# Kernel optimization log

Measured on AMD Instinct MI355X. Metric: run time of the kernel, lower is better.

Reference implementation:

```python
import jax, jax.numpy as jnp
import numpy as np
from jax import lax

N_NODES = 100000
N_EDGES = 6400000


def setup_inputs() -> dict:
    key = jax.random.key(0)
    k1, k2, k3, k4 = jax.random.split(key, 4)
    values = jax.random.uniform(k1, (N_NODES,), dtype=jnp.float32)
    edge_weights = jax.random.normal(k2, (N_EDGES,), dtype=jnp.float32)
    neighbor_idx = jax.random.randint(k3, (N_EDGES,), 0, N_NODES, dtype=jnp.int64 if jax.config.jax_enable_x64 else jnp.int32)
    segment_ids = jnp.sort(jax.random.randint(k4, (N_EDGES,), 0, N_NODES, dtype=jnp.int64 if jax.config.jax_enable_x64 else jnp.int32))
    return {
        "values": values,
        "edge_weights": edge_weights,
        "neighbor_idx": neighbor_idx,
        "segment_ids": segment_ids,
        "n_times": 3,
    }


def reference(values, edge_weights, neighbor_idx, segment_ids, n_times):
    # One forward_once: for each node i, new[i] = sigmoid(sum_{e: dst(e)=i} w_e * values[src(e)])
    # (per-node Linear(num_links, 1, bias=False) + Sigmoid, flattened over the ragged edge list)
    n_nodes = values.shape[0]

    def step(v, _):
        msgs = edge_weights * v[neighbor_idx]                      # [n_edges]
        agg = jax.ops.segment_sum(msgs, segment_ids, num_segments=n_nodes)
        return jax.nn.sigmoid(agg), None

    out, _ = lax.scan(step, values, None, length=int(n_times))
    return out
```

## Files before the change

kernel.cpp:

```cpp
#include <hip/hip_runtime.h>
#include <hip/hip_bf16.h>

#define BLK    512
#define EPT    8
#define CHUNK  12288
#define NPASS  9
#define CAP    (NPASS * CHUNK)
#define ROUNDS 3
#define SLOTS  640

__device__ __forceinline__ ushort f32_to_bf16_rne(float f) {
    unsigned u = __float_as_uint(f);
    unsigned r = (u + 0x7fffu + ((u >> 16) & 1u)) >> 16;
    return (ushort)r;
}

__global__ __launch_bounds__(BLK) void ppgcn_step(const ushort* __restrict__ vb,
                                                  const float* __restrict__ w,
                                                  const int* __restrict__ idx,
                                                  const int* __restrict__ seg,
                                                  float* __restrict__ acc,
                                                  int n_edges, int n_nodes) {
    __shared__ __align__(16) ushort chunk[2][CHUNK];
    __shared__ float slots[SLOTS];
    __shared__ int s_first, s_last;

    const int tid = threadIdx.x;
    const long long bstart = (long long)blockIdx.x * (BLK * EPT);
    const long long base   = bstart + (long long)tid * EPT;

    int ii[EPT]; float ww[EPT]; int ss[EPT];

    if (base + EPT <= (long long)n_edges) {
        const int4*   ip = reinterpret_cast<const int4*>(idx + base);
        const float4* wp = reinterpret_cast<const float4*>(w + base);
        const int4*   sp = reinterpret_cast<const int4*>(seg + base);
        #pragma unroll
        for (int q = 0; q < EPT / 4; ++q) {
            int4 a = ip[q]; float4 b = wp[q]; int4 c = sp[q];
            ii[4*q+0]=a.x; ii[4*q+1]=a.y; ii[4*q+2]=a.z; ii[4*q+3]=a.w;
            ww[4*q+0]=b.x; ww[4*q+1]=b.y; ww[4*q+2]=b.z; ww[4*q+3]=b.w;
            ss[4*q+0]=c.x; ss[4*q+1]=c.y; ss[4*q+2]=c.z; ss[4*q+3]=c.w;
        }
    } else {
        #pragma unroll
        for (int j = 0; j < EPT; ++j) {
            long long e = base + j;
            bool v = e < (long long)n_edges;
            ii[j] = v ? idx[e] : 0x7fffffff;
            ww[j] = v ? w[e]   : 0.0f;
            ss[j] = v ? seg[e] : 0x7fffffff;
        }
    }

    for (int s = tid; s < SLOTS; s += BLK) slots[s] = 0.0f;
    if (tid == 0) s_first = ss[0];
    {
        long long lastE = ((bstart + BLK * EPT) < (long long)n_edges ?
                           (bstart + BLK * EPT) : (long long)n_edges) - 1;
        int rel   = (int)(lastE - bstart);
        int owner = rel / EPT;
        int jl    = rel % EPT;
        if (tid == owner) s_last = ss[jl];
    }

    float g[EPT];
    #pragma unroll
    for (int j = 0; j < EPT; ++j) g[j] = 0.0f;

    {
        const char* gsrc = (const char*)vb;
        char* ldst = (char*)chunk[0];
        #pragma unroll
        for (int rr = 0; rr < ROUNDS; ++rr) {
            int off = (rr * BLK + tid) * 16;
            __builtin_amdgcn_global_load_lds(
                (const __attribute__((address_space(1))) void*)(gsrc + off),
                (__attribute__((address_space(3))) void*)(ldst + off),
                16, 0, 0);
        }
    }
    __syncthreads();
    const int first = s_first;

    int cur = 0;
    for (int p = 0; p < NPASS; ++p) {
        if (p + 1 < NPASS) {
            const char* gsrc = (const char*)vb + (size_t)(p + 1) * (CHUNK * 2);
            char* ldst = (char*)chunk[cur ^ 1];
            #pragma unroll
            for (int rr = 0; rr < ROUNDS; ++rr) {
                int off = (rr * BLK + tid) * 16;
                __builtin_amdgcn_global_load_lds(
                    (const __attribute__((address_space(1))) void*)(gsrc + off),
                    (__attribute__((address_space(3))) void*)(ldst + off),
                    16, 0, 0);
            }
        }

        const unsigned lo = (unsigned)(p * CHUNK);
        const ushort* cbuf = chunk[cur];
        #pragma unroll
        for (int j = 0; j < EPT; ++j) {
            unsigned rel = (unsigned)ii[j] - lo;
            if (rel < (unsigned)CHUNK) {
                unsigned u = (unsigned)cbuf[rel] << 16;
                g[j] = ww[j] * __uint_as_float(u);
            }
        }

        __syncthreads();
        cur ^= 1;
    }

    {
        float run = g[0]; int cn = ss[0];
        #pragma unroll
        for (int j = 1; j < EPT; ++j) {
            if (ss[j] != cn) {
                if ((unsigned)cn < (unsigned)n_nodes) {
                    unsigned rs = (unsigned)(cn - first);
                    if (rs < (unsigned)SLOTS) atomicAdd(&slots[rs], run);
                    else                      unsafeAtomicAdd(&acc[cn], run);
                }
                cn = ss[j]; run = g[j];
            } else {
                run += g[j];
            }
        }
        if ((unsigned)cn < (unsigned)n_nodes) {
            unsigned rs = (unsigned)(cn - first);
            if (rs < (unsigned)SLOTS) atomicAdd(&slots[rs], run);
            else                      unsafeAtomicAdd(&acc[cn], run);
        }
    }
    __syncthreads();

    {
        const int last = s_last;
        const int span = last - first;
        for (int s = tid; s <= span && s < SLOTS; s += BLK) {
            float v = slots[s];
            int node = first + s;
            if (s == 0 || node == last) unsafeAtomicAdd(&acc[node], v);
            else                        acc[node] = v;
        }
    }
}

__global__ __launch_bounds__(256) void ppgcn_convert(const float* __restrict__ src,
                                                     ushort* __restrict__ dst,
                                                     int n, int cap) {
    int i = blockIdx.x * 256 + threadIdx.x;
    if (i < cap) dst[i] = (i < n) ? f32_to_bf16_rne(src[i]) : (ushort)0;
}

__global__ __launch_bounds__(256) void ppgcn_sigmoid(float* __restrict__ acc,
                                                     ushort* __restrict__ bfout,
                                                     float* __restrict__ fout,
                                                     int n, int cap, int write_f32) {
    int i = blockIdx.x * 256 + threadIdx.x;
    if (i >= cap) return;
    if (i < n) {
        float a = acc[i];
        float s = 1.0f / (1.0f + expf(-a));
        bfout[i] = f32_to_bf16_rne(s);
        if (write_f32) fout[i] = s;
        acc[i] = 0.0f;
    } else {
        bfout[i] = 0;
    }
}

extern "C" void kernel_launch(void* const* d_in, const int* in_sizes, int n_in,
                              void* d_out, int out_size, void* d_ws, size_t ws_size,
                              hipStream_t stream) {
    const float* values       = (const float*)d_in[0];
    const float* edge_weights = (const float*)d_in[1];
    const int*   neighbor_idx = (const int*)d_in[2];
    const int*   segment_ids  = (const int*)d_in[3];

    const int n_nodes = in_sizes[0];
    const int n_edges = in_sizes[1];

    char* ws = (char*)d_ws;
    size_t abytes = ((size_t)n_nodes * sizeof(float) + 255) & ~(size_t)255;
    size_t vbytes = ((size_t)CAP * sizeof(ushort) + 255) & ~(size_t)255;
    float*  acc = (float*)ws;
    ushort* vb0 = (ushort*)(ws + abytes);
    ushort* vb1 = (ushort*)(ws + abytes + vbytes);
    ushort* vb2 = (ushort*)(ws + abytes + 2 * vbytes);
    float*  out = (float*)d_out;

    hipMemsetAsync(acc, 0, (size_t)n_nodes * sizeof(float), stream);

    int eblocks = (int)(((long long)n_edges + BLK * EPT - 1) / (BLK * EPT));
    int cblocks = (CAP + 255) / 256;

    ppgcn_convert<<<cblocks, 256, 0, stream>>>(values, vb0, n_nodes, CAP);

    ppgcn_step<<<eblocks, BLK, 0, stream>>>(vb0, edge_weights, neighbor_idx,
                                            segment_ids, acc, n_edges, n_nodes);
    ppgcn_sigmoid<<<cblocks, 256, 0, stream>>>(acc, vb1, out, n_nodes, CAP, 0);

    ppgcn_step<<<eblocks, BLK, 0, stream>>>(vb1, edge_weights, neighbor_idx,
                                            segment_ids, acc, n_edges, n_nodes);
    ppgcn_sigmoid<<<cblocks, 256, 0, stream>>>(acc, vb2, out, n_nodes, CAP, 0);

    ppgcn_step<<<eblocks, BLK, 0, stream>>>(vb2, edge_weights, neighbor_idx,
                                            segment_ids, acc, n_edges, n_nodes);
    ppgcn_sigmoid<<<cblocks, 256, 0, stream>>>(acc, vb0, out, n_nodes, CAP, 1);
}
```

Baseline: 132.1 us.

## Use smaller chunks with triple-buffered LDS prefetch and vmcnt-based waits

Shrinks the staged bf16 value chunk from 12288 to 4096 entries and switches from double to triple buffering, prefetching two chunks ahead. Each thread now issues one async global-to-LDS load per pass. A pass waits on the vmcnt counter plus a raw s_barrier instead of a full __syncthreads. Total LDS per block drops, which lets more blocks reside per CU (launch bounds now ask for 8), at the cost of 25 passes and barriers instead of 9.

Measured after the change: 183.6 us. 39.0% more time.

```diff
diff --git a/kernel.cpp b/kernel.cpp
--- a/kernel.cpp
+++ b/kernel.cpp
@@ -3,10 +3,10 @@
 
 #define BLK    512
 #define EPT    8
-#define CHUNK  12288
-#define NPASS  9
+#define CHUNK  4096
+#define NBUF   3
+#define NPASS  25
 #define CAP    (NPASS * CHUNK)
-#define ROUNDS 3
 #define SLOTS  640
 
 __device__ __forceinline__ ushort f32_to_bf16_rne(float f) {
@@ -15,13 +15,13 @@
     return (ushort)r;
 }
 
-__global__ __launch_bounds__(BLK) void ppgcn_step(const ushort* __restrict__ vb,
-                                                  const float* __restrict__ w,
-                                                  const int* __restrict__ idx,
-                                                  const int* __restrict__ seg,
-                                                  float* __restrict__ acc,
-                                                  int n_edges, int n_nodes) {
-    __shared__ __align__(16) ushort chunk[2][CHUNK];
+__global__ __launch_bounds__(BLK, 8) void ppgcn_step(const ushort* __restrict__ vb,
+                                                     const float* __restrict__ w,
+                                                     const int* __restrict__ idx,
+                                                     const int* __restrict__ seg,
+                                                     float* __restrict__ acc,
+                                                     int n_edges, int n_nodes) {
+    __shared__ __align__(16) ushort chunk[NBUF][CHUNK];
     __shared__ float slots[SLOTS];
     __shared__ int s_first, s_last;
 
@@ -68,38 +68,42 @@
     #pragma unroll
     for (int j = 0; j < EPT; ++j) g[j] = 0.0f;
 
-    {
-        const char* gsrc = (const char*)vb;
-        char* ldst = (char*)chunk[0];
-        #pragma unroll
-        for (int rr = 0; rr < ROUNDS; ++rr) {
-            int off = (rr * BLK + tid) * 16;
-            __builtin_amdgcn_global_load_lds(
-                (const __attribute__((address_space(1))) void*)(gsrc + off),
-                (__attribute__((address_space(3))) void*)(ldst + off),
-                16, 0, 0);
-        }
+    const int my_off = tid * 16;
+
+    {
+        const char* g0 = (const char*)vb + my_off;
+        const char* g1 = (const char*)vb + (size_t)(CHUNK * 2) + my_off;
+        __builtin_amdgcn_global_load_lds(
+            (const __attribute__((address_space(1))) void*)g0,
+            (__attribute__((address_space(3))) void*)((char*)chunk[0] + my_off),
+            16, 0, 0);
+        __builtin_amdgcn_global_load_lds(
+            (const __attribute__((address_space(1))) void*)g1,
+            (__attribute__((address_space(3))) void*)((char*)chunk[1] + my_off),
+            16, 0, 0);
     }
     __syncthreads();
     const int first = s_first;
 
-    int cur = 0;
     for (int p = 0; p < NPASS; ++p) {
-        if (p + 1 < NPASS) {
-            const char* gsrc = (const char*)vb + (size_t)(p + 1) * (CHUNK * 2);
-            char* ldst = (char*)chunk[cur ^ 1];
-            #pragma unroll
-            for (int rr = 0; rr < ROUNDS; ++rr) {
-                int off = (rr * BLK + tid) * 16;
-                __builtin_amdgcn_global_load_lds(
-                    (const __attribute__((address_space(1))) void*)(gsrc + off),
-                    (__attribute__((address_space(3))) void*)(ldst + off),
-                    16, 0, 0);
-            }
+        if (p > 0) {
+            if (p == NPASS - 1) asm volatile("s_waitcnt vmcnt(0)" ::: "memory");
+            else                asm volatile("s_waitcnt vmcnt(1)" ::: "memory");
+            __builtin_amdgcn_s_barrier();
+            __builtin_amdgcn_sched_barrier(0);
+        }
+
+        if (p + 2 < NPASS) {
+            const char* gs = (const char*)vb + (size_t)(p + 2) * (CHUNK * 2) + my_off;
+            char* ld = (char*)chunk[(p + 2) % NBUF] + my_off;
+            __builtin_amdgcn_global_load_lds(
+                (const __attribute__((address_space(1))) void*)gs,
+                (__attribute__((address_space(3))) void*)ld,
+                16, 0, 0);
         }
 
         const unsigned lo = (unsigned)(p * CHUNK);
-        const ushort* cbuf = chunk[cur];
+        const ushort* cbuf = chunk[p % NBUF];
         #pragma unroll
         for (int j = 0; j < EPT; ++j) {
             unsigned rel = (unsigned)ii[j] - lo;
@@ -108,9 +112,6 @@
                 g[j] = ww[j] * __uint_as_float(u);
             }
         }
-
-        __syncthreads();
-        cur ^= 1;
     }
 
     {
```

## Replace LDS-staged bf16 value chunks with direct fp32 global gathers

Applied to the files above, without the earlier changes.

Drops the per-block loop that streamed the whole bf16 value table through double-buffered LDS in nine passes. Each edge now gathers its fp32 value straight from global memory, relying on the small table staying resident in L2. This also removes the bf16 conversion kernel and moves to a 256-thread block with a smaller slot array. The sigmoid kernel is vectorised to float4. The trade is many random L2 gathers in place of bulk table copies into LDS in every block.

Measured after the change: 115.0 us. -13.0%, faster.

```diff
diff --git a/kernel.cpp b/kernel.cpp
--- a/kernel.cpp
+++ b/kernel.cpp
@@ -1,27 +1,16 @@
 #include <hip/hip_runtime.h>
 #include <hip/hip_bf16.h>
 
-#define BLK    512
+#define BLK    256
 #define EPT    8
-#define CHUNK  12288
-#define NPASS  9
-#define CAP    (NPASS * CHUNK)
-#define ROUNDS 3
-#define SLOTS  640
+#define SLOTS  384
 
-__device__ __forceinline__ ushort f32_to_bf16_rne(float f) {
-    unsigned u = __float_as_uint(f);
-    unsigned r = (u + 0x7fffu + ((u >> 16) & 1u)) >> 16;
-    return (ushort)r;
-}
-
-__global__ __launch_bounds__(BLK) void ppgcn_step(const ushort* __restrict__ vb,
-                                                  const float* __restrict__ w,
-                                                  const int* __restrict__ idx,
-                                                  const int* __restrict__ seg,
-                                                  float* __restrict__ acc,
-                                                  int n_edges, int n_nodes) {
-    __shared__ __align__(16) ushort chunk[2][CHUNK];
+__global__ __launch_bounds__(BLK, 8) void ppgcn_step(const float* __restrict__ v,
+                                                     const float* __restrict__ w,
+                                                     const int* __restrict__ idx,
+                                                     const int* __restrict__ seg,
+                                                     float* __restrict__ acc,
+                                                     int n_edges, int n_nodes) {
     __shared__ float slots[SLOTS];
     __shared__ int s_first, s_last;
 
@@ -37,21 +26,33 @@
         const int4*   sp = reinterpret_cast<const int4*>(seg + base);
         #pragma unroll
         for (int q = 0; q < EPT / 4; ++q) {
-            int4 a = ip[q]; float4 b = wp[q]; int4 c = sp[q];
+            int4 a = ip[q];
             ii[4*q+0]=a.x; ii[4*q+1]=a.y; ii[4*q+2]=a.z; ii[4*q+3]=a.w;
+        }
+        #pragma unroll
+        for (int q = 0; q < EPT / 4; ++q) {
+            float4 b = wp[q];
             ww[4*q+0]=b.x; ww[4*q+1]=b.y; ww[4*q+2]=b.z; ww[4*q+3]=b.w;
+        }
+        #pragma unroll
+        for (int q = 0; q < EPT / 4; ++q) {
+            int4 c = sp[q];
             ss[4*q+0]=c.x; ss[4*q+1]=c.y; ss[4*q+2]=c.z; ss[4*q+3]=c.w;
         }
     } else {
         #pragma unroll
         for (int j = 0; j < EPT; ++j) {
             long long e = base + j;
-            bool v = e < (long long)n_edges;
-            ii[j] = v ? idx[e] : 0x7fffffff;
-            ww[j] = v ? w[e]   : 0.0f;
-            ss[j] = v ? seg[e] : 0x7fffffff;
+            bool val = e < (long long)n_edges;
+            ii[j] = val ? idx[e] : 0;
+            ww[j] = val ? w[e]   : 0.0f;
+            ss[j] = val ? seg[e] : 0x7fffffff;
         }
     }
+
+    float g[EPT];
+    #pragma unroll
+    for (int j = 0; j < EPT; ++j) g[j] = v[ii[j]];
 
     for (int s = tid; s < SLOTS; s += BLK) slots[s] = 0.0f;
     if (tid == 0) s_first = ss[0];
@@ -63,55 +64,11 @@
         int jl    = rel % EPT;
         if (tid == owner) s_last = ss[jl];
     }
-
-    float g[EPT];
-    #pragma unroll
-    for (int j = 0; j < EPT; ++j) g[j] = 0.0f;
-
-    {
-        const char* gsrc = (const char*)vb;
-        char* ldst = (char*)chunk[0];
-        #pragma unroll
-        for (int rr = 0; rr < ROUNDS; ++rr) {
-            int off = (rr * BLK + tid) * 16;
-            __builtin_amdgcn_global_load_lds(
-                (const __attribute__((address_space(1))) void*)(gsrc + off),
-                (__attribute__((address_space(3))) void*)(ldst + off),
-                16, 0, 0);
-        }
-    }
     __syncthreads();
     const int first = s_first;
 
-    int cur = 0;
-    for (int p = 0; p < NPASS; ++p) {
-        if (p + 1 < NPASS) {
-            const char* gsrc = (const char*)vb + (size_t)(p + 1) * (CHUNK * 2);
-            char* ldst = (char*)chunk[cur ^ 1];
-            #pragma unroll
-            for (int rr = 0; rr < ROUNDS; ++rr) {
-                int off = (rr * BLK + tid) * 16;
-                __builtin_amdgcn_global_load_lds(
-                    (const __attribute__((address_space(1))) void*)(gsrc + off),
-                    (__attribute__((address_space(3))) void*)(ldst + off),
-                    16, 0, 0);
-            }
-        }
-
-        const unsigned lo = (unsigned)(p * CHUNK);
-        const ushort* cbuf = chunk[cur];
-        #pragma unroll
-        for (int j = 0; j < EPT; ++j) {
-            unsigned rel = (unsigned)ii[j] - lo;
-            if (rel < (unsigned)CHUNK) {
-                unsigned u = (unsigned)cbuf[rel] << 16;
-                g[j] = ww[j] * __uint_as_float(u);
-            }
-        }
-
-        __syncthreads();
-        cur ^= 1;
-    }
+    #pragma unroll
+    for (int j = 0; j < EPT; ++j) g[j] *= ww[j];
 
     {
         float run = g[0]; int cn = ss[0];
@@ -140,35 +97,36 @@
         const int last = s_last;
         const int span = last - first;
         for (int s = tid; s <= span && s < SLOTS; s += BLK) {
-            float v = slots[s];
+            float val = slots[s];
             int node = first + s;
-            if (s == 0 || node == last) unsafeAtomicAdd(&acc[node], v);
-            else                        acc[node] = v;
+            if (s == 0 || node == last) unsafeAtomicAdd(&acc[node], val);
+            else                        acc[node] = val;
         }
     }
 }
 
-__global__ __launch_bounds__(256) void ppgcn_convert(const float* __restrict__ src,
-                                                     ushort* __restrict__ dst,
-                                                     int n, int cap) {
-    int i = blockIdx.x * 256 + threadIdx.x;
-    if (i < cap) dst[i] = (i < n) ? f32_to_bf16_rne(src[i]) : (ushort)0;
-}
-
 __global__ __launch_bounds__(256) void ppgcn_sigmoid(float* __restrict__ acc,
-                                                     ushort* __restrict__ bfout,
+                                                     float* __restrict__ vnext,
                                                      float* __restrict__ fout,
-                                                     int n, int cap, int write_f32) {
-    int i = blockIdx.x * 256 + threadIdx.x;
-    if (i >= cap) return;
-    if (i < n) {
-        float a = acc[i];
-        float s = 1.0f / (1.0f + expf(-a));
-        bfout[i] = f32_to_bf16_rne(s);
-        if (write_f32) fout[i] = s;
-        acc[i] = 0.0f;
+                                                     int n, int write_f32) {
+    int i = (blockIdx.x * 256 + threadIdx.x) * 4;
+    if (i + 4 <= n) {
+        float4 a = *reinterpret_cast<float4*>(&acc[i]);
+        float4 r;
+        r.x = 1.0f / (1.0f + expf(-a.x));
+        r.y = 1.0f / (1.0f + expf(-a.y));
+        r.z = 1.0f / (1.0f + expf(-a.z));
+        r.w = 1.0f / (1.0f + expf(-a.w));
+        *reinterpret_cast<float4*>(&vnext[i]) = r;
+        if (write_f32) *reinterpret_cast<float4*>(&fout[i]) = r;
+        *reinterpret_cast<float4*>(&acc[i]) = make_float4(0.f, 0.f, 0.f, 0.f);
     } else {
-        bfout[i] = 0;
+        for (int k = i; k < n; ++k) {
+            float s = 1.0f / (1.0f + expf(-acc[k]));
+            vnext[k] = s;
+            if (write_f32) fout[k] = s;
+            acc[k] = 0.0f;
+        }
     }
 }
 
@@ -185,29 +143,25 @@
 
     char* ws = (char*)d_ws;
     size_t abytes = ((size_t)n_nodes * sizeof(float) + 255) & ~(size_t)255;
-    size_t vbytes = ((size_t)CAP * sizeof(ushort) + 255) & ~(size_t)255;
-    float*  acc = (float*)ws;
-    ushort* vb0 = (ushort*)(ws + abytes);
-    ushort* vb1 = (ushort*)(ws + abytes + vbytes);
-    ushort* vb2 = (ushort*)(ws + abytes + 2 * vbytes);
-    float*  out = (float*)d_out;
+    float* acc  = (float*)ws;
+    float* bufA = (float*)(ws + abytes);
+    float* bufB = (float*)(ws + 2 * abytes);
+    float* out  = (float*)d_out;
 
     hipMemsetAsync(acc, 0, (size_t)n_nodes * sizeof(float), stream);
 
     int eblocks = (int)(((long long)n_edges + BLK * EPT - 1) / (BLK * EPT));
-    int cblocks = (CAP + 255) / 256;
+    int nblocks = (n_nodes + 4 * 256 - 1) / (4 * 256);
 
-    ppgcn_convert<<<cblocks, 256, 0, stream>>>(values, vb0, n_nodes, CAP);
+    ppgcn_step<<<eblocks, BLK, 0, stream>>>(values, edge_weights, neighbor_idx,
+                                            segment_ids, acc, n_edges, n_nodes);
+    ppgcn_sigmoid<<<nblocks, 256, 0, stream>>>(acc, bufA, out, n_nodes, 0);
 
-    ppgcn_step<<<eblocks, BLK, 0, stream>>>(vb0, edge_weights, neighbor_idx,
+    ppgcn_step<<<eblocks, BLK, 0, stream>>>(bufA, edge_weights, neighbor_idx,
                                             segment_ids, acc, n_edges, n_nodes);
-    ppgcn_sigmoid<<<cblocks, 256, 0, stream>>>(acc, vb1, out, n_nodes, CAP, 0);
+    ppgcn_sigmoid<<<nblocks, 256, 0, stream>>>(acc, bufB, out, n_nodes, 0);
 
-    ppgcn_step<<<eblocks, BLK, 0, stream>>>(vb1, edge_weights, neighbor_idx,
+    ppgcn_step<<<eblocks, BLK, 0, stream>>>(bufB, edge_weights, neighbor_idx,
                                             segment_ids, acc, n_edges, n_nodes);
-    ppgcn_sigmoid<<<cblocks, 256, 0, stream>>>(acc, vb2, out, n_nodes, CAP, 0);
-
-    ppgcn_step<<<eblocks, BLK, 0, stream>>>(vb2, edge_weights, neighbor_idx,
-                                            segment_ids, acc, n_edges, n_nodes);
-    ppgcn_sigmoid<<<cblocks, 256, 0, stream>>>(acc, vb0, out, n_nodes, CAP, 1);
+    ppgcn_sigmoid<<<nblocks, 256, 0, stream>>>(acc, bufB, out, n_nodes, 1);
 }
```
